# Kernel tuning notes

Hardware: AMD Instinct MI355X
Metric: run time of the kernel (lower is better)

The kernel has to match this reference:

```python
import jax, jax.numpy as jnp
import numpy as np

EPS = 1e-12

def setup_inputs() -> dict:
    key = jax.random.key(0)
    ks = jax.random.split(key, 7)
    bs, seq, d_in, d_out = 8, 2048, 4096, 4096
    n_tasks, n_splits, n_skills, rank = 64, 1, 8, 16
    return {
        "x": jax.random.normal(ks[0], (bs, seq, d_in), dtype=jnp.float32),
        "weight": jax.random.normal(ks[1], (d_out, d_in), dtype=jnp.float32) * 0.02,
        "bias": jax.random.normal(ks[2], (d_out,), dtype=jnp.float32) * 0.02,
        "module_logits": jax.random.normal(ks[3], (n_tasks, n_splits * n_skills), dtype=jnp.float32) * 0.001,
        "lora_a": jax.random.normal(ks[4], (n_splits, n_skills, d_in // n_splits, rank), dtype=jnp.float32) * 0.02,
        "lora_b": jax.random.normal(ks[5], (n_splits, n_skills, rank, d_out // n_splits), dtype=jnp.float32) * 0.02,
        "task_ids": jax.random.randint(ks[6], (bs,), 0, n_tasks, dtype=jnp.int64),
    }

def reference(x, weight, bias, module_logits, lora_a, lora_b, task_ids):
    # Eval-mode PolytroponSelector: sigmoid then sum-normalize per split.
    n_splits, n_skills, _, rank = lora_a.shape
    bs = x.shape[0]
    mw = jax.nn.sigmoid(module_logits[task_ids]).reshape(bs, n_splits, n_skills)
    mw = mw / (mw.sum(axis=-1, keepdims=True) + EPS)
    # Mix per-skill LoRA factors: A [bs, in, rank], B [bs, rank, out]
    A = jnp.einsum('bqs,qsdr->bqdr', mw, lora_a).reshape(bs, -1, rank)
    B = jnp.einsum('bqs,qsrd->bqrd', mw, lora_b)
    B = jnp.transpose(B, (0, 2, 1, 3)).reshape(bs, rank, -1)
    # Low-rank adapter path: (x @ A) @ B / rank
    adapter = jnp.einsum('btr,bro->bto', jnp.einsum('bti,bir->btr', x, A), B) / rank
    # Base linear + adapter
    return jnp.einsum('bti,oi->bto', x, weight) + bias + adapter
```

## Files before the change

kernel.cpp:

```cpp
#include <hip/hip_runtime.h>
#include <hip/hip_bf16.h>
#include <cstdint>
#include <cstddef>

typedef __attribute__((ext_vector_type(4))) float floatx4;
typedef __attribute__((ext_vector_type(8))) __bf16 bf16x8;

#define BS 8
#define SEQ 2048
#define M_TOT 16384
#define DK 4096
#define DN 4096
#define NSK 8
#define RANK 16

__device__ __forceinline__ unsigned short f2bf(float f) {
  union { __hip_bfloat16 h; unsigned short u; } v;
  v.h = __float2bfloat16(f);
  return v.u;
}

__device__ __forceinline__ void async16(const void* g, void* l) {
  __builtin_amdgcn_global_load_lds(
      (const __attribute__((address_space(1))) unsigned int*)g,
      (__attribute__((address_space(3))) unsigned int*)l, 16, 0, 0);
}

__global__ void prep_mw_kernel(const float* __restrict__ logits,
                               const void* __restrict__ task_raw,
                               float* __restrict__ mw) {
  const int* t32 = (const int*)task_raw;
  bool is64 = true;
#pragma unroll
  for (int b = 0; b < BS; ++b)
    if (t32[2 * b + 1] != 0) is64 = false;
  int tid = threadIdx.x;
  int b = tid >> 3, s = tid & 7;
  int task = is64 ? t32[2 * b] : t32[b];
  float lg = logits[task * NSK + s];
  float sg = 1.0f / (1.0f + expf(-lg));
  float sum = sg;
  sum += __shfl_xor(sum, 1);
  sum += __shfl_xor(sum, 2);
  sum += __shfl_xor(sum, 4);
  mw[tid] = sg / (sum + 1e-12f);
}

__global__ __launch_bounds__(256) void prep_a_kernel(
    const float* __restrict__ lora_a, const float* __restrict__ mw,
    unsigned short* __restrict__ a_bft) {
  int b = blockIdx.y;
  int d = blockIdx.x * 256 + threadIdx.x;
  float w[NSK];
#pragma unroll
  for (int s = 0; s < NSK; ++s) w[s] = mw[b * NSK + s];
  float acc[RANK];
#pragma unroll
  for (int r = 0; r < RANK; ++r) acc[r] = 0.f;
  for (int s = 0; s < NSK; ++s) {
    const float4* p = (const float4*)&lora_a[((size_t)s * DK + d) * RANK];
#pragma unroll
    for (int q = 0; q < 4; ++q) {
      float4 v = p[q];
      acc[q * 4 + 0] += w[s] * v.x;
      acc[q * 4 + 1] += w[s] * v.y;
      acc[q * 4 + 2] += w[s] * v.z;
      acc[q * 4 + 3] += w[s] * v.w;
    }
  }
#pragma unroll
  for (int r = 0; r < RANK; ++r)
    a_bft[((size_t)b * RANK + r) * DK + d] = f2bf(acc[r]);
}

__global__ __launch_bounds__(256) void prep_b_kernel(
    const float* __restrict__ lora_b, const float* __restrict__ mw,
    unsigned short* __restrict__ baug) {
  int b = blockIdx.y;
  int n = blockIdx.x * 256 + threadIdx.x;
  float w[NSK];
#pragma unroll
  for (int s = 0; s < NSK; ++s) w[s] = mw[b * NSK + s];
  unsigned short ov[32];
#pragma unroll
  for (int r = 0; r < RANK; ++r) {
    float acc = 0.f;
#pragma unroll
    for (int s = 0; s < NSK; ++s)
      acc += w[s] * lora_b[((size_t)s * RANK + r) * DN + n];
    ov[r] = f2bf(acc * 0.0625f);
  }
#pragma unroll
  for (int r = RANK; r < 32; ++r) ov[r] = 0;
  uint4* dst = (uint4*)&baug[((size_t)b * DN + n) * 32];
  const uint4* sv = (const uint4*)ov;
  dst[0] = sv[0]; dst[1] = sv[1]; dst[2] = sv[2]; dst[3] = sv[3];
}

__global__ __launch_bounds__(256) void conv_f32_to_bf16(
    const float* __restrict__ src, unsigned short* __restrict__ dst,
    long long n4) {
  long long stride = (long long)gridDim.x * 256;
  for (long long i = (long long)blockIdx.x * 256 + threadIdx.x; i < n4; i += stride) {
    float4 v = ((const float4*)src)[i];
    ushort4 o;
    o.x = f2bf(v.x); o.y = f2bf(v.y); o.z = f2bf(v.z); o.w = f2bf(v.w);
    ((ushort4*)dst)[i] = o;
  }
}

__global__ __launch_bounds__(256) void t_gemm_kernel(
    const unsigned short* __restrict__ xb, const unsigned short* __restrict__ abft,
    float* __restrict__ t_f32) {
  const int wave = threadIdx.x >> 6;
  const int lane = threadIdx.x & 63;
  const int mtile = blockIdx.x * 4 + wave;
  const int row0 = mtile * 16;
  const int b = row0 >> 11;
  const int k0 = blockIdx.y * 1024;
  const int fr = lane & 15;
  const int fq = (lane >> 4) * 8;
  const unsigned short* pa = xb + (size_t)(row0 + fr) * DK + fq + k0;
  const unsigned short* pb = abft + ((size_t)b * RANK + fr) * DK + fq + k0;
  floatx4 acc = {0.f, 0.f, 0.f, 0.f};
  for (int k = 0; k < 1024; k += 32) {
    bf16x8 av = *(const bf16x8*)(pa + k);
    bf16x8 bv = *(const bf16x8*)(pb + k);
    acc = __builtin_amdgcn_mfma_f32_16x16x32_bf16(av, bv, acc, 0, 0, 0);
  }
  const int col = lane & 15;
  const int rowq = (lane >> 4) * 4;
#pragma unroll
  for (int j = 0; j < 4; ++j)
    atomicAdd(&t_f32[(size_t)(row0 + rowq + j) * RANK + col], acc[j]);
}

__global__ __launch_bounds__(256) void t_final_kernel(
    const float* __restrict__ t_f32, unsigned short* __restrict__ taug) {
  int i = blockIdx.x * 256 + threadIdx.x;
  int row = i >> 4, r = i & 15;
  taug[(size_t)row * 32 + r] = f2bf(t_f32[i]);
  taug[(size_t)row * 32 + 16 + r] = 0;
}

__global__ __launch_bounds__(256) void main_gemm(
    const unsigned short* __restrict__ xb, const unsigned short* __restrict__ wb,
    const unsigned short* __restrict__ taug, const unsigned short* __restrict__ baug,
    const float* __restrict__ bias, float* __restrict__ out) {
  __shared__ __align__(16) unsigned short sA[128 * 32];
  __shared__ __align__(16) unsigned short sB[128 * 32];
  const int tid = threadIdx.x;
  const int wave = tid >> 6;
  const int lane = tid & 63;
  const int bx = blockIdx.x, by = blockIdx.y;
  const int m0 = by * 128, n0 = bx * 128;
  const int batch = by >> 4;

  const int srow = lane >> 2;
  const int skk = (lane & 3) * 8;
  const int rA0 = wave * 16 + srow;
  const int rA1 = rA0 + 64;
  const unsigned short* gA0 = xb + (size_t)(m0 + rA0) * DK + skk;
  const unsigned short* gA1 = xb + (size_t)(m0 + rA1) * DK + skk;
  const unsigned short* gB0 = wb + (size_t)(n0 + rA0) * DK + skk;
  const unsigned short* gB1 = wb + (size_t)(n0 + rA1) * DK + skk;
  const unsigned short* gA0x = taug + (size_t)(m0 + rA0) * 32 + skk;
  const unsigned short* gA1x = taug + (size_t)(m0 + rA1) * 32 + skk;
  const unsigned short* gB0x = baug + ((size_t)batch * DN + n0 + rA0) * 32 + skk;
  const unsigned short* gB1x = baug + ((size_t)batch * DN + n0 + rA1) * 32 + skk;
  unsigned short* lA0 = sA + wave * 512;
  unsigned short* lA1 = sA + (wave + 4) * 512;
  unsigned short* lB0 = sB + wave * 512;
  unsigned short* lB1 = sB + (wave + 4) * 512;

  floatx4 acc[4][4];
#pragma unroll
  for (int i = 0; i < 4; ++i)
#pragma unroll
    for (int j = 0; j < 4; ++j) acc[i][j] = (floatx4){0.f, 0.f, 0.f, 0.f};

  const int wm = (wave >> 1) * 64;
  const int wn = (wave & 1) * 64;
  const int fr = lane & 15;
  const int fq = (lane >> 4) * 8;

  for (int s = 0; s < 129; ++s) {
    __syncthreads();
    if (s < 128) {
      const int k0 = s * 32;
      async16(gA0 + k0, lA0);
      async16(gA1 + k0, lA1);
      async16(gB0 + k0, lB0);
      async16(gB1 + k0, lB1);
    } else {
      async16(gA0x, lA0);
      async16(gA1x, lA1);
      async16(gB0x, lB0);
      async16(gB1x, lB1);
    }
    __syncthreads();

    bf16x8 av[4], bv[4];
#pragma unroll
    for (int t = 0; t < 4; ++t) {
      av[t] = *(const bf16x8*)&sA[(wm + t * 16 + fr) * 32 + fq];
      bv[t] = *(const bf16x8*)&sB[(wn + t * 16 + fr) * 32 + fq];
    }
#pragma unroll
    for (int tm = 0; tm < 4; ++tm)
#pragma unroll
      for (int tn = 0; tn < 4; ++tn)
        acc[tm][tn] = __builtin_amdgcn_mfma_f32_16x16x32_bf16(av[tm], bv[tn],
                                                              acc[tm][tn], 0, 0, 0);
  }

  const int colt = lane & 15;
  const int rowq = (lane >> 4) * 4;
#pragma unroll
  for (int tn = 0; tn < 4; ++tn) {
    const int col = n0 + wn + tn * 16 + colt;
    const float bvv = bias[col];
#pragma unroll
    for (int tm = 0; tm < 4; ++tm) {
      const size_t row = (size_t)(m0 + wm + tm * 16 + rowq);
      float* po = out + row * DN + col;
#pragma unroll
      for (int j = 0; j < 4; ++j) po[(size_t)j * DN] = acc[tm][tn][j] + bvv;
    }
  }
}

extern "C" void kernel_launch(void* const* d_in, const int* in_sizes, int n_in,
                              void* d_out, int out_size, void* d_ws, size_t ws_size,
                              hipStream_t stream) {
  (void)in_sizes; (void)n_in; (void)out_size; (void)ws_size;
  const float* x             = (const float*)d_in[0];
  const float* weight        = (const float*)d_in[1];
  const float* bias          = (const float*)d_in[2];
  const float* module_logits = (const float*)d_in[3];
  const float* lora_a        = (const float*)d_in[4];
  const float* lora_b        = (const float*)d_in[5];
  const void*  task_ids      = d_in[6];
  float* out = (float*)d_out;

  char* ws = (char*)d_ws;
  unsigned short* xb   = (unsigned short*)(ws);
  unsigned short* wb   = (unsigned short*)(ws + 134217728);
  unsigned short* taug = (unsigned short*)(ws + 167772160);
  unsigned short* baug = (unsigned short*)(ws + 168820736);
  unsigned short* abft = (unsigned short*)(ws + 170917888);
  float*          tf32 = (float*)(ws + 171966464);
  float*          mw   = (float*)(ws + 173015040);

  hipLaunchKernelGGL(prep_mw_kernel, dim3(1), dim3(64), 0, stream,
                     module_logits, task_ids, mw);
  hipLaunchKernelGGL(prep_a_kernel, dim3(16, 8), dim3(256), 0, stream,
                     lora_a, mw, abft);
  hipLaunchKernelGGL(prep_b_kernel, dim3(16, 8), dim3(256), 0, stream,
                     lora_b, mw, baug);
  hipLaunchKernelGGL(conv_f32_to_bf16, dim3(2048), dim3(256), 0, stream,
                     weight, wb, (long long)(4096LL * 4096 / 4));
  hipLaunchKernelGGL(conv_f32_to_bf16, dim3(8192), dim3(256), 0, stream,
                     x, xb, (long long)(16384LL * 4096 / 4));
  hipMemsetAsync(tf32, 0, (size_t)M_TOT * RANK * sizeof(float), stream);
  hipLaunchKernelGGL(t_gemm_kernel, dim3(256, 4), dim3(256), 0, stream,
                     xb, abft, tf32);
  hipLaunchKernelGGL(t_final_kernel, dim3(1024), dim3(256), 0, stream,
                     tf32, taug);
  hipLaunchKernelGGL(main_gemm, dim3(32, 128), dim3(256), 0, stream,
                     xb, wb, taug, baug, bias, out);
}
```

Measured before the change: 1.195 ms.

## Rewrite main GEMM with 256x256 tiles, double-buffered LDS pipeline and swizzle

Replaces the 128x128 single-buffered main GEMM with a 256x256 tile per 512-thread block. It uses a 128KB double-buffered LDS ring with XOR-swizzled layout, async global-to-LDS prefetch two k-steps ahead, and interleaved ds_read/MFMA phases with s_setprio. Blocks are remapped in groups of 8 for L2 locality, and the LoRA rank-augmented term is applied after the main loop directly from global memory. The aim is to hide load latency, cut the barrier stalls of the old sync-per-k-step loop, and raise reuse per byte loaded. In exchange it adds heavy register pressure (128 accumulator floats per thread) and relies on carefully hand-counted vmcnt waits.

```diff
diff --git a/kernel.cpp b/kernel.cpp
--- a/kernel.cpp
+++ b/kernel.cpp
@@ -143,91 +143,182 @@
   taug[(size_t)row * 32 + 16 + r] = 0;
 }
 
-__global__ __launch_bounds__(256) void main_gemm(
+__global__ __launch_bounds__(512, 2) void main_gemm(
     const unsigned short* __restrict__ xb, const unsigned short* __restrict__ wb,
     const unsigned short* __restrict__ taug, const unsigned short* __restrict__ baug,
     const float* __restrict__ bias, float* __restrict__ out) {
-  __shared__ __align__(16) unsigned short sA[128 * 32];
-  __shared__ __align__(16) unsigned short sB[128 * 32];
+  __shared__ __align__(1024) unsigned short lds[65536];
+
   const int tid = threadIdx.x;
   const int wave = tid >> 6;
   const int lane = tid & 63;
-  const int bx = blockIdx.x, by = blockIdx.y;
-  const int m0 = by * 128, n0 = bx * 128;
-  const int batch = by >> 4;
-
-  const int srow = lane >> 2;
-  const int skk = (lane & 3) * 8;
-  const int rA0 = wave * 16 + srow;
-  const int rA1 = rA0 + 64;
-  const unsigned short* gA0 = xb + (size_t)(m0 + rA0) * DK + skk;
-  const unsigned short* gA1 = xb + (size_t)(m0 + rA1) * DK + skk;
-  const unsigned short* gB0 = wb + (size_t)(n0 + rA0) * DK + skk;
-  const unsigned short* gB1 = wb + (size_t)(n0 + rA1) * DK + skk;
-  const unsigned short* gA0x = taug + (size_t)(m0 + rA0) * 32 + skk;
-  const unsigned short* gA1x = taug + (size_t)(m0 + rA1) * 32 + skk;
-  const unsigned short* gB0x = baug + ((size_t)batch * DN + n0 + rA0) * 32 + skk;
-  const unsigned short* gB1x = baug + ((size_t)batch * DN + n0 + rA1) * 32 + skk;
-  unsigned short* lA0 = sA + wave * 512;
-  unsigned short* lA1 = sA + (wave + 4) * 512;
-  unsigned short* lB0 = sB + wave * 512;
-  unsigned short* lB1 = sB + (wave + 4) * 512;
-
-  floatx4 acc[4][4];
-#pragma unroll
-  for (int i = 0; i < 4; ++i)
-#pragma unroll
-    for (int j = 0; j < 4; ++j) acc[i][j] = (floatx4){0.f, 0.f, 0.f, 0.f};
-
-  const int wm = (wave >> 1) * 64;
-  const int wn = (wave & 1) * 64;
+  const int wm = wave >> 2;
+  const int wn = wave & 3;
   const int fr = lane & 15;
-  const int fq = (lane >> 4) * 8;
-
-  for (int s = 0; s < 129; ++s) {
-    __syncthreads();
-    if (s < 128) {
-      const int k0 = s * 32;
-      async16(gA0 + k0, lA0);
-      async16(gA1 + k0, lA1);
-      async16(gB0 + k0, lB0);
-      async16(gB1 + k0, lB1);
-    } else {
-      async16(gA0x, lA0);
-      async16(gA1x, lA1);
-      async16(gB0x, lB0);
-      async16(gB1x, lB1);
+  const int fq = (lane >> 4) << 3;
+  const int swz = (lane & 12) << 1;
+
+  const int orig = blockIdx.x;
+  const int swb = (orig & 7) * 128 + (orig >> 3);
+  const int tile_m = swb >> 4;
+  const int tile_n = swb & 15;
+  const int m0 = tile_m * 256;
+  const int n0 = tile_n * 256;
+  const int batch = tile_m >> 3;
+
+  const int l16 = lane << 4;
+  const int o = l16 ^ ((l16 & 512) >> 4) ^ ((l16 & 256) >> 4);
+  const int rin = o >> 6;
+  const int k2 = (o & 63) >> 1;
+  const int s0 = wave * 2, s1 = s0 + 1;
+  const unsigned short* aS0 = xb + (size_t)(m0 + (s0 & 7) * 16 + rin) * DK + (s0 >> 3) * 32 + k2;
+  const unsigned short* aS1 = xb + (size_t)(m0 + (s1 & 7) * 16 + rin) * DK + (s1 >> 3) * 32 + k2;
+  const unsigned short* bS0 = wb + (size_t)(n0 + (s0 & 7) * 16 + rin) * DK + (s0 >> 3) * 32 + k2;
+  const unsigned short* bS1 = wb + (size_t)(n0 + (s1 & 7) * 16 + rin) * DK + (s1 >> 3) * 32 + k2;
+
+#define STG_A(d, h, kt) do {                                                        \
+    async16(aS0 + (((size_t)(h)) << 19) + ((size_t)(kt) << 6),                      \
+            &lds[(d) * 32768 + (h) * 8192 + s0 * 512]);                             \
+    async16(aS1 + (((size_t)(h)) << 19) + ((size_t)(kt) << 6),                      \
+            &lds[(d) * 32768 + (h) * 8192 + s1 * 512]);                             \
+  } while (0)
+#define STG_B(d, h, kt) do {                                                        \
+    async16(bS0 + (((size_t)(h)) << 19) + ((size_t)(kt) << 6),                      \
+            &lds[(d) * 32768 + 16384 + (h) * 8192 + s0 * 512]);                     \
+    async16(bS1 + (((size_t)(h)) << 19) + ((size_t)(kt) << 6),                      \
+            &lds[(d) * 32768 + 16384 + (h) * 8192 + s1 * 512]);                     \
+  } while (0)
+
+#define RD_A(d, t, ks)                                                              \
+  (*(const bf16x8*)&lds[(((d) * 32768) + wm * 8192 + (ks) * 4096 +                  \
+                         ((t) * 16 + fr) * 32 + fq) ^ swz])
+#define RD_B(d, u, ks)                                                              \
+  (*(const bf16x8*)&lds[(((d) * 32768) + 16384 + (wn >> 1) * 8192 + (ks) * 4096 +   \
+                         ((wn & 1) * 64 + (u) * 16 + fr) * 32 + fq) ^ swz])
+
+  floatx4 acc[8][4];
+#pragma unroll
+  for (int t = 0; t < 8; ++t)
+#pragma unroll
+    for (int u = 0; u < 4; ++u) acc[t][u] = (floatx4){0.f, 0.f, 0.f, 0.f};
+
+  bf16x8 a[4][2];
+  bf16x8 b0[2][2];
+  bf16x8 b1[2][2];
+
+  STG_A(0, 0, 0); STG_A(0, 1, 0); STG_B(0, 0, 0); STG_B(0, 1, 0);
+  STG_A(1, 0, 1); STG_A(1, 1, 1); STG_B(1, 0, 1);
+  asm volatile("s_waitcnt vmcnt(6)" ::: "memory");
+  __builtin_amdgcn_s_barrier();
+
+#define TILE(d, kt) do {                                                            \
+                      \
+    _Pragma("unroll")                                                               \
+    for (int t = 0; t < 4; ++t) { a[t][0] = RD_A(d, t, 0); a[t][1] = RD_A(d, t, 1); } \
+    _Pragma("unroll")                                                               \
+    for (int u = 0; u < 2; ++u) { b0[u][0] = RD_B(d, u, 0); b0[u][1] = RD_B(d, u, 1); } \
+    if ((kt) + 1 < 64) STG_B(1 - (d), 1, (kt) + 1);                                 \
+    __builtin_amdgcn_s_barrier();                                                   \
+    asm volatile("s_waitcnt lgkmcnt(0)" ::: "memory");                              \
+    __builtin_amdgcn_s_setprio(1);                                                  \
+    _Pragma("unroll")                                                               \
+    for (int t = 0; t < 4; ++t)                                                     \
+      _Pragma("unroll")                                                             \
+      for (int u = 0; u < 2; ++u) {                                                 \
+        acc[t][u] = __builtin_amdgcn_mfma_f32_16x16x32_bf16(a[t][0], b0[u][0], acc[t][u], 0, 0, 0); \
+        acc[t][u] = __builtin_amdgcn_mfma_f32_16x16x32_bf16(a[t][1], b0[u][1], acc[t][u], 0, 0, 0); \
+      }                                                                             \
+    __builtin_amdgcn_s_setprio(0);                                                  \
+    __builtin_amdgcn_s_barrier();                                                   \
+                                             \
+    _Pragma("unroll")                                                               \
+    for (int u = 0; u < 2; ++u) { b1[u][0] = RD_B(d, u + 2, 0); b1[u][1] = RD_B(d, u + 2, 1); } \
+    __builtin_amdgcn_s_barrier();                                                   \
+    asm volatile("s_waitcnt lgkmcnt(0)" ::: "memory");                              \
+    __builtin_amdgcn_s_setprio(1);                                                  \
+    _Pragma("unroll")                                                               \
+    for (int t = 0; t < 4; ++t)                                                     \
+      _Pragma("unroll")                                                             \
+      for (int u = 0; u < 2; ++u) {                                                 \
+        acc[t][u + 2] = __builtin_amdgcn_mfma_f32_16x16x32_bf16(a[t][0], b1[u][0], acc[t][u + 2], 0, 0, 0); \
+        acc[t][u + 2] = __builtin_amdgcn_mfma_f32_16x16x32_bf16(a[t][1], b1[u][1], acc[t][u + 2], 0, 0, 0); \
+      }                                                                             \
+    __builtin_amdgcn_s_setprio(0);                                                  \
+    __builtin_amdgcn_s_barrier();                                                   \
+                                             \
+    _Pragma("unroll")                                                               \
+    for (int t = 0; t < 4; ++t) { a[t][0] = RD_A(d, t + 4, 0); a[t][1] = RD_A(d, t + 4, 1); } \
+    __builtin_amdgcn_s_barrier();                                                   \
+    asm volatile("s_waitcnt lgkmcnt(0)" ::: "memory");                              \
+    __builtin_amdgcn_s_setprio(1);                                                  \
+    _Pragma("unroll")                                                               \
+    for (int t = 0; t < 4; ++t)                                                     \
+      _Pragma("unroll")                                                             \
+      for (int u = 0; u < 2; ++u) {                                                 \
+        acc[t + 4][u] = __builtin_amdgcn_mfma_f32_16x16x32_bf16(a[t][0], b0[u][0], acc[t + 4][u], 0, 0, 0); \
+        acc[t + 4][u] = __builtin_amdgcn_mfma_f32_16x16x32_bf16(a[t][1], b0[u][1], acc[t + 4][u], 0, 0, 0); \
+      }                                                                             \
+    __builtin_amdgcn_s_setprio(0);                                                  \
+    __builtin_amdgcn_s_barrier();                                                   \
+         \
+        \
+    if ((kt) + 2 < 64) {                                                            \
+      STG_A(d, 0, (kt) + 2); STG_A(d, 1, (kt) + 2); STG_B(d, 0, (kt) + 2);          \
+      asm volatile("s_waitcnt vmcnt(6)" ::: "memory");                              \
+    } else {                                                                        \
+      asm volatile("s_waitcnt vmcnt(0)" ::: "memory");                              \
+    }                                                                               \
+    __builtin_amdgcn_s_barrier();                                                   \
+    __builtin_amdgcn_s_setprio(1);                                                  \
+    _Pragma("unroll")                                                               \
+    for (int t = 0; t < 4; ++t)                                                     \
+      _Pragma("unroll")                                                             \
+      for (int u = 0; u < 2; ++u) {                                                 \
+        acc[t + 4][u + 2] = __builtin_amdgcn_mfma_f32_16x16x32_bf16(a[t][0], b1[u][0], acc[t + 4][u + 2], 0, 0, 0); \
+        acc[t + 4][u + 2] = __builtin_amdgcn_mfma_f32_16x16x32_bf16(a[t][1], b1[u][1], acc[t + 4][u + 2], 0, 0, 0); \
+      }                                                                             \
+    __builtin_amdgcn_s_setprio(0);                                                  \
+    __builtin_amdgcn_s_barrier();                                                   \
+  } while (0)
+
+  for (int it = 0; it < 32; ++it) {
+    const int kt0 = it * 2;
+    TILE(0, kt0);
+    TILE(1, kt0 + 1);
+  }
+
+  {
+    const unsigned short* tA = taug + (size_t)(m0 + wm * 128 + fr) * 32 + fq;
+    const unsigned short* tB = baug + ((size_t)batch * DN + n0 + wn * 64 + fr) * 32 + fq;
+    bf16x8 av[8], bv[4];
+#pragma unroll
+    for (int t = 0; t < 8; ++t) av[t] = *(const bf16x8*)(tA + (size_t)t * 512);
+#pragma unroll
+    for (int u = 0; u < 4; ++u) bv[u] = *(const bf16x8*)(tB + (size_t)u * 512);
+#pragma unroll
+    for (int t = 0; t < 8; ++t)
+#pragma unroll
+      for (int u = 0; u < 4; ++u)
+        acc[t][u] = __builtin_amdgcn_mfma_f32_16x16x32_bf16(av[t], bv[u], acc[t][u], 0, 0, 0);
+  }
+
+  const int rowq = (lane >> 4) * 4;
+#pragma unroll
+  for (int u = 0; u < 4; ++u) {
+    const int col = n0 + wn * 64 + u * 16 + fr;
+    const float bvv = bias[col];
+#pragma unroll
+    for (int t = 0; t < 8; ++t) {
+      float* po = out + (size_t)(m0 + wm * 128 + t * 16 + rowq) * DN + col;
+#pragma unroll
+      for (int j = 0; j < 4; ++j) po[(size_t)j * DN] = acc[t][u][j] + bvv;
     }
-    __syncthreads();
-
-    bf16x8 av[4], bv[4];
-#pragma unroll
-    for (int t = 0; t < 4; ++t) {
-      av[t] = *(const bf16x8*)&sA[(wm + t * 16 + fr) * 32 + fq];
-      bv[t] = *(const bf16x8*)&sB[(wn + t * 16 + fr) * 32 + fq];
-    }
-#pragma unroll
-    for (int tm = 0; tm < 4; ++tm)
-#pragma unroll
-      for (int tn = 0; tn < 4; ++tn)
-        acc[tm][tn] = __builtin_amdgcn_mfma_f32_16x16x32_bf16(av[tm], bv[tn],
-                                                              acc[tm][tn], 0, 0, 0);
-  }
-
-  const int colt = lane & 15;
-  const int rowq = (lane >> 4) * 4;
-#pragma unroll
-  for (int tn = 0; tn < 4; ++tn) {
-    const int col = n0 + wn + tn * 16 + colt;
-    const float bvv = bias[col];
-#pragma unroll
-    for (int tm = 0; tm < 4; ++tm) {
-      const size_t row = (size_t)(m0 + wm + tm * 16 + rowq);
-      float* po = out + row * DN + col;
-#pragma unroll
-      for (int j = 0; j < 4; ++j) po[(size_t)j * DN] = acc[tm][tn][j] + bvv;
-    }
-  }
+  }
+#undef TILE
+#undef RD_A
+#undef RD_B
+#undef STG_A
+#undef STG_B
 }
 
 extern "C" void kernel_launch(void* const* d_in, const int* in_sizes, int n_in,
@@ -267,6 +358,6 @@
                      xb, abft, tf32);
   hipLaunchKernelGGL(t_final_kernel, dim3(1024), dim3(256), 0, stream,
                      tf32, taug);
-  hipLaunchKernelGGL(main_gemm, dim3(32, 128), dim3(256), 0, stream,
+  hipLaunchKernelGGL(main_gemm, dim3(1024), dim3(512), 0, stream,
                      xb, wb, taug, baug, bias, out);
 }
```

Measured after the change: 1.179 ms. Within noise of the previous version (-1.3%).
